# Performance work log

Measured on AMD Instinct MI355X. Metric: run time of the kernel, lower is better.

The kernel has to match this reference:

```python
import jax, jax.numpy as jnp
import numpy as np

TAU = 0.07          # temperature
NUM_CLASSES = 1000  # label vocabulary size (used for bincount length)


def setup_inputs() -> dict:
    key = jax.random.key(0)
    kq, kk, ky = jax.random.split(key, 3)
    N, K, D = 8192, 8, 512
    q = jax.random.normal(kq, (N, D), dtype=jnp.float32)
    q = q / jnp.linalg.norm(q, axis=1, keepdims=True)          # L2-normalized anchors
    k = jax.random.normal(kk, (N, K, D), dtype=jnp.float32)
    k = k / jnp.linalg.norm(k, axis=2, keepdims=True)          # L2-normalized positives
    y = jax.random.randint(ky, (N,), 0, NUM_CLASSES, dtype=jnp.int32)
    return {"q": q, "k": k, "y": y}


def reference(q, k, y):
    # q: [N, D] anchors, k: [N, K, D] external positives, y: [N] labels
    N, K, D = k.shape
    neg_inf = jnp.float32(-jnp.inf)

    # similarities to external positives and within-batch, scaled by temperature
    k_sims = jnp.einsum('nd,nkd->nk', q, k) / TAU            # [N, K]
    batch_sims = jnp.matmul(q, q.T) / TAU                    # [N, N]

    same = y[:, None] == y[None, :]                          # [N, N] label equality
    eye = jnp.eye(N, dtype=bool)
    same_class_mask = same & ~eye                            # in-batch positives (excl. self)
    same_class_counts = same_class_mask.sum(axis=1) + K      # [N]

    # faithful to torch: multiply by mask then masked_fill(x == 0, -inf)
    batch_pos = batch_sims * same_class_mask
    batch_pos = jnp.where(batch_pos == 0, neg_inf, batch_pos)
    pos_sims = jnp.concatenate([k_sims, batch_pos], axis=1)  # [N, K+N]
    num = jax.scipy.special.logsumexp(pos_sims, axis=1)      # [N]

    y_counts = jnp.bincount(y, length=NUM_CLASSES)           # [C]
    neg_sims = batch_sims * (~same)
    neg_sims = jnp.where(neg_sims == 0, neg_inf, neg_sims)
    # class-frequency-weighted denominator (as in the original, no max-shift)
    den = jnp.log(jnp.sum(jnp.exp(neg_sims) / y_counts[y][None, :].astype(q.dtype), axis=1))

    loss = -(num - den) / same_class_counts.astype(q.dtype)
    return loss.mean()
```

## Files before the change

kernel.cpp:

```cpp
#include <hip/hip_runtime.h>
#include <hip/hip_fp8.h>
#include <stdint.h>

constexpr int N    = 8192;
constexpr int D    = 512;
constexpr int KEXT = 8;
constexpr int NCLS = 1000;
#define TAU_INV  14.285714285714285714f
#define SQRT_TI  3.7796447300922722f

typedef long   long2_t __attribute__((ext_vector_type(2)));
typedef float  f32x4   __attribute__((ext_vector_type(4)));

typedef __attribute__((address_space(1))) void gvoid;
typedef __attribute__((address_space(3))) void lvoid;

__device__ __forceinline__ uint32_t pack4_e4m3(float a, float b, float c, float d) {
    __hip_fp8_e4m3 A(a), B(b), C(c), D(d);
    return (uint32_t)A.__x | ((uint32_t)B.__x << 8) |
           ((uint32_t)C.__x << 16) | ((uint32_t)D.__x << 24);
}

__global__ void prep_k(const float* __restrict__ q, const int* __restrict__ y,
                       uint32_t* __restrict__ qf8, int* __restrict__ counts,
                       float* __restrict__ invy, float* __restrict__ pos,
                       float* __restrict__ neg) {
    const int b = blockIdx.x, tid = threadIdx.x;
    if (b == 0) {
        __shared__ int h[NCLS];
        for (int i = tid; i < NCLS; i += 256) h[i] = 0;
        __syncthreads();
        for (int i = tid; i < N; i += 256) atomicAdd(&h[y[i]], 1);
        __syncthreads();
        for (int i = tid; i < NCLS; i += 256) counts[i] = h[i];
        for (int i = tid; i < N; i += 256) invy[i] = 1.0f / (float)h[y[i]];
        return;
    }
    const int gid = (b - 1) * 256 + tid;
    const int row = gid >> 5;
    const int c   = gid & 31;
    const int ks2 = c >> 2, quad = c & 3;
    const float* src = q + (size_t)row * D + ks2 * 64 + quad * 8;
    float4 v0 = *reinterpret_cast<const float4*>(src);
    float4 v1 = *reinterpret_cast<const float4*>(src + 4);
    float4 v2 = *reinterpret_cast<const float4*>(src + 32);
    float4 v3 = *reinterpret_cast<const float4*>(src + 36);
    uint4 o;
    o.x = pack4_e4m3(v0.x * SQRT_TI, v0.y * SQRT_TI, v0.z * SQRT_TI, v0.w * SQRT_TI);
    o.y = pack4_e4m3(v1.x * SQRT_TI, v1.y * SQRT_TI, v1.z * SQRT_TI, v1.w * SQRT_TI);
    o.z = pack4_e4m3(v2.x * SQRT_TI, v2.y * SQRT_TI, v2.z * SQRT_TI, v2.w * SQRT_TI);
    o.w = pack4_e4m3(v3.x * SQRT_TI, v3.y * SQRT_TI, v3.z * SQRT_TI, v3.w * SQRT_TI);
    const int t = row >> 4, l15 = row & 15;
    reinterpret_cast<uint4*>(qf8)[(size_t)t * 512 + ks2 * 64 + quad * 16 + l15] = o;
    if (gid < N) { pos[gid] = 0.f; neg[gid] = 0.f; }
}

__global__ __launch_bounds__(256, 2) void gemm_k(
        const uint32_t* __restrict__ qf8,
        const int* __restrict__ y,
        const float* __restrict__ invy,
        float* __restrict__ pos_sum,
        float* __restrict__ neg_sum) {
    __shared__ long2_t Asl[4096];
    __shared__ int   yR[128];
    __shared__ float redP[2][128];
    __shared__ float redN[2][128];

    const int tid  = threadIdx.x;
    const int wave = tid >> 6;
    const int lane = tid & 63;
    const int quad = lane >> 4;
    const int l15  = lane & 15;

    const int ib     = blockIdx.x >> 3;
    const int jchunk = blockIdx.x & 7;
    const int ibase  = ib * 128;

    {
        const uint32_t* src = qf8 + (size_t)ib * 16384;
#pragma unroll
        for (int it = 0; it < 16; it++) {
            const int idx = it * 256 + tid;
            __builtin_amdgcn_global_load_lds((gvoid*)(src + idx * 4),
                                             (lvoid*)(Asl + idx), 16, 0, 0);
        }
    }
    if (tid < 128) yR[tid] = y[ibase + tid];
    __syncthreads();

    const int wr = (wave >> 1) * 64;
    const int wc = (wave & 1) * 64;
    const int half = wave & 1;

    float posp[16], negp[16];
#pragma unroll
    for (int e = 0; e < 16; e++) { posp[e] = 0.f; negp[e] = 0.f; }

    const long2_t* fb = reinterpret_cast<const long2_t*>(qf8);
    const long2_t* pB[4];
#pragma unroll
    for (int m = 0; m < 4; m++)
        pB[m] = fb + (size_t)(jchunk * 64 + (wc >> 4) + m) * 512 + lane;

    const long2_t* As = Asl + (wr >> 4) * 512 + lane;

    for (int jt = 0; jt < 8; jt++) {
        const int j0 = jchunk * 1024 + jt * 128;

        int   yjv[4];
        float icj[4];
#pragma unroll
        for (int mj = 0; mj < 4; mj++) {
            int jc = j0 + wc + mj * 16 + l15;
            yjv[mj] = y[jc];
            icj[mj] = invy[jc];
        }

        f32x4 acc[4][4];
#pragma unroll
        for (int a = 0; a < 4; a++)
#pragma unroll
            for (int c = 0; c < 4; c++) acc[a][c] = (f32x4)0.0f;

        long2_t bf[2][4];
#pragma unroll
        for (int m = 0; m < 4; m++) bf[0][m] = pB[m][0];

#pragma unroll
        for (int ks2 = 0; ks2 < 8; ks2++) {
            const int cur = ks2 & 1, nxt = cur ^ 1;
            if (ks2 < 7) {
#pragma unroll
                for (int m = 0; m < 4; m++) bf[nxt][m] = pB[m][(ks2 + 1) * 64];
            }
            long2_t af[4];
#pragma unroll
            for (int m = 0; m < 4; m++) af[m] = As[m * 512 + ks2 * 64];
#pragma unroll
            for (int mi = 0; mi < 4; mi++)
#pragma unroll
                for (int mj = 0; mj < 4; mj++)
                    acc[mi][mj] = __builtin_amdgcn_mfma_f32_16x16x32_fp8_fp8(
                        af[mi].x, bf[cur][mj].x, acc[mi][mj], 0, 0, 0);
#pragma unroll
            for (int mi = 0; mi < 4; mi++)
#pragma unroll
                for (int mj = 0; mj < 4; mj++)
                    acc[mi][mj] = __builtin_amdgcn_mfma_f32_16x16x32_fp8_fp8(
                        af[mi].y, bf[cur][mj].y, acc[mi][mj], 0, 0, 0);
        }
#pragma unroll
        for (int m = 0; m < 4; m++) pB[m] += 4096;

#pragma unroll
        for (int mi = 0; mi < 4; mi++) {
#pragma unroll
            for (int r = 0; r < 4; r++) {
                const int il   = wr + mi * 16 + quad * 4 + r;
                const int irow = ibase + il;
                const int myi  = yR[il];
                float ps = 0.f, ns = 0.f;
#pragma unroll
                for (int mj = 0; mj < 4; mj++) {
                    const int jcol = j0 + wc + mj * 16 + l15;
                    float a    = acc[mi][mj][r];
                    float ex   = __expf(a);
                    bool  nz   = (a != 0.0f);
                    bool  same = (myi == yjv[mj]);
                    ps += (same && (irow != jcol) && nz) ? ex : 0.0f;
                    ns += (!same && nz) ? ex * icj[mj] : 0.0f;
                }
                posp[mi * 4 + r] += ps;
                negp[mi * 4 + r] += ns;
            }
        }
    }

#pragma unroll
    for (int mi = 0; mi < 4; mi++) {
#pragma unroll
        for (int r = 0; r < 4; r++) {
            const int e = mi * 4 + r;
            float ps = posp[e], ns = negp[e];
#pragma unroll
            for (int off = 1; off < 16; off <<= 1) {
                ps += __shfl_xor(ps, off);
                ns += __shfl_xor(ns, off);
            }
            if (l15 == 0) {
                const int il = wr + mi * 16 + quad * 4 + r;
                redP[half][il] = ps;
                redN[half][il] = ns;
            }
        }
    }
    __syncthreads();
    if (tid < 128) {
        atomicAdd(&pos_sum[ibase + tid], redP[0][tid] + redP[1][tid]);
    } else if (tid < 256) {
        const int il = tid - 128;
        atomicAdd(&neg_sum[ibase + il], redN[0][il] + redN[1][il]);
    }
}

__global__ void finalize_k(const float* __restrict__ q, const float* __restrict__ kmat,
                           const int* __restrict__ y, const int* __restrict__ counts,
                           const float* __restrict__ pos_sum, const float* __restrict__ neg_sum,
                           float* __restrict__ loss) {
    const int wave = threadIdx.x >> 6, lane = threadIdx.x & 63;
    const int i = blockIdx.x * 4 + wave;

    const float4* q4 = reinterpret_cast<const float4*>(q) + (size_t)i * 128;
    const float4* k4 = reinterpret_cast<const float4*>(kmat) + (size_t)i * KEXT * 128;
    float4 qa = q4[lane], qb = q4[lane + 64];

    float esum = 0.f;
    for (int kk = 0; kk < KEXT; kk++) {
        float4 ka = k4[(size_t)kk * 128 + lane];
        float4 kb = k4[(size_t)kk * 128 + lane + 64];
        float p = qa.x * ka.x;
        p = fmaf(qa.y, ka.y, p); p = fmaf(qa.z, ka.z, p); p = fmaf(qa.w, ka.w, p);
        p = fmaf(qb.x, kb.x, p); p = fmaf(qb.y, kb.y, p);
        p = fmaf(qb.z, kb.z, p); p = fmaf(qb.w, kb.w, p);
#pragma unroll
        for (int off = 1; off < 64; off <<= 1) p += __shfl_xor(p, off);
        esum += __expf(p * TAU_INV);
    }
    if (lane == 0) {
        float num = logf(esum + pos_sum[i]);
        float den = logf(neg_sum[i]);
        float cnt = (float)(counts[y[i]] - 1 + KEXT);
        loss[i] = -(num - den) / cnt;
    }
}

__global__ void reduce_k(const float* __restrict__ loss, float* __restrict__ out) {
    __shared__ float part[16];
    int tid = threadIdx.x;
    float s = 0.f;
    for (int i = tid; i < N; i += 1024) s += loss[i];
#pragma unroll
    for (int off = 1; off < 64; off <<= 1) s += __shfl_xor(s, off);
    if ((tid & 63) == 0) part[tid >> 6] = s;
    __syncthreads();
    if (tid < 16) {
        float v = part[tid];
#pragma unroll
        for (int off = 1; off < 16; off <<= 1) v += __shfl_xor(v, off);
        if (tid == 0) out[0] = v / (float)N;
    }
}

extern "C" void kernel_launch(void* const* d_in, const int* in_sizes, int n_in,
                              void* d_out, int out_size, void* d_ws, size_t ws_size,
                              hipStream_t stream) {
    const float* q    = (const float*)d_in[0];
    const float* kmat = (const float*)d_in[1];
    const int*   y    = (const int*)d_in[2];
    float* out = (float*)d_out;

    char* ws = (char*)d_ws;
    uint32_t* qf8  = (uint32_t*)ws;
    int*   counts  = (int*)  (ws + 4194304);
    float* invy    = (float*)(ws + 4198400);
    float* pos     = (float*)(ws + 4231168);
    float* neg     = (float*)(ws + 4263936);
    float* loss    = (float*)(ws + 4296704);

    prep_k    <<<1 + (N * 32) / 256, 256, 0, stream>>>(q, y, qf8, counts, invy, pos, neg);
    gemm_k    <<<512, 256, 0, stream>>>(qf8, y, invy, pos, neg);
    finalize_k<<<N / 4, 256, 0, stream>>>(q, kmat, y, counts, pos, neg, loss);
    reduce_k  <<<1, 1024, 0, stream>>>(loss, out);
}
```

Baseline: 333.1 us.

## Move same-class positive sums out of GEMM epilogue into sparse finalize pass

The GEMM epilogue now sums every off-diagonal exp weighted by inverse class count, with no label compares and no positive accumulator. Finalize ballots over the labels to find each row's same-class partners and computes their positive similarities in fp32. It also recomputes their fp8 dot products so it can subtract those terms from the negative sum. Adds a deeper register prefetch ring in the GEMM and folds the mean reduction into finalize with an atomic, which drops one launch. The risks are a scan of all 8192 labels per row in finalize and floating-point cancellation in the subtraction.

```diff
diff --git a/kernel.cpp b/kernel.cpp
--- a/kernel.cpp
+++ b/kernel.cpp
@@ -20,11 +20,14 @@
     return (uint32_t)A.__x | ((uint32_t)B.__x << 8) |
            ((uint32_t)C.__x << 16) | ((uint32_t)D.__x << 24);
 }
+__device__ __forceinline__ float f8tof(uint32_t b) {
+    __hip_fp8_e4m3 v; v.__x = (uint8_t)b; return (float)v;
+}
 
 __global__ void prep_k(const float* __restrict__ q, const int* __restrict__ y,
                        uint32_t* __restrict__ qf8, int* __restrict__ counts,
-                       float* __restrict__ invy, float* __restrict__ pos,
-                       float* __restrict__ neg) {
+                       float* __restrict__ invy, float* __restrict__ neg,
+                       float* __restrict__ out) {
     const int b = blockIdx.x, tid = threadIdx.x;
     if (b == 0) {
         __shared__ int h[NCLS];
@@ -33,6 +36,7 @@
         for (int i = tid; i < N; i += 256) atomicAdd(&h[y[i]], 1);
         __syncthreads();
         for (int i = tid; i < NCLS; i += 256) counts[i] = h[i];
+        if (tid == 0) out[0] = 0.f;
         for (int i = tid; i < N; i += 256) invy[i] = 1.0f / (float)h[y[i]];
         return;
     }
@@ -52,18 +56,14 @@
     o.w = pack4_e4m3(v3.x * SQRT_TI, v3.y * SQRT_TI, v3.z * SQRT_TI, v3.w * SQRT_TI);
     const int t = row >> 4, l15 = row & 15;
     reinterpret_cast<uint4*>(qf8)[(size_t)t * 512 + ks2 * 64 + quad * 16 + l15] = o;
-    if (gid < N) { pos[gid] = 0.f; neg[gid] = 0.f; }
+    if (gid < N) neg[gid] = 0.f;
 }
 
 __global__ __launch_bounds__(256, 2) void gemm_k(
         const uint32_t* __restrict__ qf8,
-        const int* __restrict__ y,
         const float* __restrict__ invy,
-        float* __restrict__ pos_sum,
         float* __restrict__ neg_sum) {
     __shared__ long2_t Asl[4096];
-    __shared__ int   yR[128];
-    __shared__ float redP[2][128];
     __shared__ float redN[2][128];
 
     const int tid  = threadIdx.x;
@@ -85,16 +85,15 @@
                                              (lvoid*)(Asl + idx), 16, 0, 0);
         }
     }
-    if (tid < 128) yR[tid] = y[ibase + tid];
     __syncthreads();
 
     const int wr = (wave >> 1) * 64;
     const int wc = (wave & 1) * 64;
     const int half = wave & 1;
 
-    float posp[16], negp[16];
-#pragma unroll
-    for (int e = 0; e < 16; e++) { posp[e] = 0.f; negp[e] = 0.f; }
+    float negp[16];
+#pragma unroll
+    for (int e = 0; e < 16; e++) negp[e] = 0.f;
 
     const long2_t* fb = reinterpret_cast<const long2_t*>(qf8);
     const long2_t* pB[4];
@@ -107,13 +106,12 @@
     for (int jt = 0; jt < 8; jt++) {
         const int j0 = jchunk * 1024 + jt * 128;
 
-        int   yjv[4];
+        int   jc[4];
         float icj[4];
 #pragma unroll
         for (int mj = 0; mj < 4; mj++) {
-            int jc = j0 + wc + mj * 16 + l15;
-            yjv[mj] = y[jc];
-            icj[mj] = invy[jc];
+            jc[mj]  = j0 + wc + mj * 16 + l15;
+            icj[mj] = invy[jc[mj]];
         }
 
         f32x4 acc[4][4];
@@ -122,32 +120,38 @@
 #pragma unroll
             for (int c = 0; c < 4; c++) acc[a][c] = (f32x4)0.0f;
 
-        long2_t bf[2][4];
-#pragma unroll
-        for (int m = 0; m < 4; m++) bf[0][m] = pB[m][0];
-
+        long2_t bf[3][4], af[2][4];
+#pragma unroll
+        for (int m = 0; m < 4; m++) {
+            bf[0][m] = pB[m][0];
+            bf[1][m] = pB[m][64];
+            af[0][m] = As[m * 512];
+        }
 #pragma unroll
         for (int ks2 = 0; ks2 < 8; ks2++) {
-            const int cur = ks2 & 1, nxt = cur ^ 1;
+            const int cur = ks2 % 3;
+            if (ks2 + 2 < 8) {
+                const int ns = (ks2 + 2) % 3;
+#pragma unroll
+                for (int m = 0; m < 4; m++) bf[ns][m] = pB[m][(ks2 + 2) * 64];
+            }
+            const int ac = ks2 & 1;
             if (ks2 < 7) {
 #pragma unroll
-                for (int m = 0; m < 4; m++) bf[nxt][m] = pB[m][(ks2 + 1) * 64];
-            }
-            long2_t af[4];
-#pragma unroll
-            for (int m = 0; m < 4; m++) af[m] = As[m * 512 + ks2 * 64];
+                for (int m = 0; m < 4; m++) af[ac ^ 1][m] = As[m * 512 + (ks2 + 1) * 64];
+            }
 #pragma unroll
             for (int mi = 0; mi < 4; mi++)
 #pragma unroll
                 for (int mj = 0; mj < 4; mj++)
                     acc[mi][mj] = __builtin_amdgcn_mfma_f32_16x16x32_fp8_fp8(
-                        af[mi].x, bf[cur][mj].x, acc[mi][mj], 0, 0, 0);
+                        af[ac][mi].x, bf[cur][mj].x, acc[mi][mj], 0, 0, 0);
 #pragma unroll
             for (int mi = 0; mi < 4; mi++)
 #pragma unroll
                 for (int mj = 0; mj < 4; mj++)
                     acc[mi][mj] = __builtin_amdgcn_mfma_f32_16x16x32_fp8_fp8(
-                        af[mi].y, bf[cur][mj].y, acc[mi][mj], 0, 0, 0);
+                        af[ac][mi].y, bf[cur][mj].y, acc[mi][mj], 0, 0, 0);
         }
 #pragma unroll
         for (int m = 0; m < 4; m++) pB[m] += 4096;
@@ -156,21 +160,14 @@
         for (int mi = 0; mi < 4; mi++) {
 #pragma unroll
             for (int r = 0; r < 4; r++) {
-                const int il   = wr + mi * 16 + quad * 4 + r;
-                const int irow = ibase + il;
-                const int myi  = yR[il];
-                float ps = 0.f, ns = 0.f;
+                const int irow = ibase + wr + mi * 16 + quad * 4 + r;
+                float ns = 0.f;
 #pragma unroll
                 for (int mj = 0; mj < 4; mj++) {
-                    const int jcol = j0 + wc + mj * 16 + l15;
-                    float a    = acc[mi][mj][r];
-                    float ex   = __expf(a);
-                    bool  nz   = (a != 0.0f);
-                    bool  same = (myi == yjv[mj]);
-                    ps += (same && (irow != jcol) && nz) ? ex : 0.0f;
-                    ns += (!same && nz) ? ex * icj[mj] : 0.0f;
+                    float ex = __expf(acc[mi][mj][r]);
+                    ex = (irow == jc[mj]) ? 0.f : ex;
+                    ns = fmaf(ex, icj[mj], ns);
                 }
-                posp[mi * 4 + r] += ps;
                 negp[mi * 4 + r] += ns;
             }
         }
@@ -180,44 +177,34 @@
     for (int mi = 0; mi < 4; mi++) {
 #pragma unroll
         for (int r = 0; r < 4; r++) {
-            const int e = mi * 4 + r;
-            float ps = posp[e], ns = negp[e];
-#pragma unroll
-            for (int off = 1; off < 16; off <<= 1) {
-                ps += __shfl_xor(ps, off);
-                ns += __shfl_xor(ns, off);
-            }
-            if (l15 == 0) {
-                const int il = wr + mi * 16 + quad * 4 + r;
-                redP[half][il] = ps;
-                redN[half][il] = ns;
-            }
+            float ns = negp[mi * 4 + r];
+#pragma unroll
+            for (int off = 1; off < 16; off <<= 1) ns += __shfl_xor(ns, off);
+            if (l15 == 0) redN[half][wr + mi * 16 + quad * 4 + r] = ns;
         }
     }
     __syncthreads();
-    if (tid < 128) {
-        atomicAdd(&pos_sum[ibase + tid], redP[0][tid] + redP[1][tid]);
-    } else if (tid < 256) {
-        const int il = tid - 128;
-        atomicAdd(&neg_sum[ibase + il], redN[0][il] + redN[1][il]);
-    }
+    if (tid < 128)
+        atomicAdd(&neg_sum[ibase + tid], redN[0][tid] + redN[1][tid]);
 }
 
 __global__ void finalize_k(const float* __restrict__ q, const float* __restrict__ kmat,
                            const int* __restrict__ y, const int* __restrict__ counts,
-                           const float* __restrict__ pos_sum, const float* __restrict__ neg_sum,
-                           float* __restrict__ loss) {
+                           const float* __restrict__ neg_sum,
+                           const uint32_t* __restrict__ qf8,
+                           float* __restrict__ out) {
+    __shared__ float part[4];
     const int wave = threadIdx.x >> 6, lane = threadIdx.x & 63;
     const int i = blockIdx.x * 4 + wave;
 
-    const float4* q4 = reinterpret_cast<const float4*>(q) + (size_t)i * 128;
+    const float4* q4 = reinterpret_cast<const float4*>(q);
+    float4 qa = q4[(size_t)i * 128 + lane], qb = q4[(size_t)i * 128 + 64 + lane];
+
     const float4* k4 = reinterpret_cast<const float4*>(kmat) + (size_t)i * KEXT * 128;
-    float4 qa = q4[lane], qb = q4[lane + 64];
-
     float esum = 0.f;
     for (int kk = 0; kk < KEXT; kk++) {
         float4 ka = k4[(size_t)kk * 128 + lane];
-        float4 kb = k4[(size_t)kk * 128 + lane + 64];
+        float4 kb = k4[(size_t)kk * 128 + 64 + lane];
         float p = qa.x * ka.x;
         p = fmaf(qa.y, ka.y, p); p = fmaf(qa.z, ka.z, p); p = fmaf(qa.w, ka.w, p);
         p = fmaf(qb.x, kb.x, p); p = fmaf(qb.y, kb.y, p);
@@ -226,29 +213,63 @@
         for (int off = 1; off < 64; off <<= 1) p += __shfl_xor(p, off);
         esum += __expf(p * TAU_INV);
     }
+
+    const uint4* f4 = reinterpret_cast<const uint4*>(qf8);
+    const bool act = lane < 32;
+    const int ks2 = lane >> 2, quad = lane & 3;
+    const size_t goff = (size_t)ks2 * 64 + quad * 16;
+    uint4 iv = act ? f4[(size_t)(i >> 4) * 512 + goff + (i & 15)] : uint4{0, 0, 0, 0};
+    float fi[16];
+#pragma unroll
+    for (int w = 0; w < 4; w++) {
+        uint32_t word = (&iv.x)[w];
+#pragma unroll
+        for (int t = 0; t < 4; t++) fi[w * 4 + t] = f8tof((word >> (8 * t)) & 0xffu);
+    }
+
+    const int myy = y[i];
+    float pos = 0.f, corr = 0.f;
+    for (int it = 0; it < 128; it++) {
+        unsigned long long m = __ballot(y[it * 64 + lane] == myy);
+        if (it == (i >> 6)) m &= ~(1ull << (i & 63));
+        while (m) {
+            const int b = __builtin_ctzll(m); m &= m - 1;
+            const int j = it * 64 + b;
+            float4 ja = q4[(size_t)j * 128 + lane], jb = q4[(size_t)j * 128 + 64 + lane];
+            float p = qa.x * ja.x;
+            p = fmaf(qa.y, ja.y, p); p = fmaf(qa.z, ja.z, p); p = fmaf(qa.w, ja.w, p);
+            p = fmaf(qb.x, jb.x, p); p = fmaf(qb.y, jb.y, p);
+            p = fmaf(qb.z, jb.z, p); p = fmaf(qb.w, jb.w, p);
+            uint4 jv = act ? f4[(size_t)(j >> 4) * 512 + goff + (j & 15)] : uint4{0, 0, 0, 0};
+            float p8 = 0.f;
+#pragma unroll
+            for (int w = 0; w < 4; w++) {
+                uint32_t word = (&jv.x)[w];
+#pragma unroll
+                for (int t = 0; t < 4; t++)
+                    p8 = fmaf(fi[w * 4 + t], f8tof((word >> (8 * t)) & 0xffu), p8);
+            }
+#pragma unroll
+            for (int off = 1; off < 64; off <<= 1) {
+                p  += __shfl_xor(p, off);
+                p8 += __shfl_xor(p8, off);
+            }
+            pos  += __expf(p * TAU_INV);
+            corr += __expf(p8);
+        }
+    }
+
     if (lane == 0) {
-        float num = logf(esum + pos_sum[i]);
-        float den = logf(neg_sum[i]);
-        float cnt = (float)(counts[y[i]] - 1 + KEXT);
-        loss[i] = -(num - den) / cnt;
-    }
-}
-
-__global__ void reduce_k(const float* __restrict__ loss, float* __restrict__ out) {
-    __shared__ float part[16];
-    int tid = threadIdx.x;
-    float s = 0.f;
-    for (int i = tid; i < N; i += 1024) s += loss[i];
-#pragma unroll
-    for (int off = 1; off < 64; off <<= 1) s += __shfl_xor(s, off);
-    if ((tid & 63) == 0) part[tid >> 6] = s;
+        const float ici = 1.0f / (float)counts[myy];
+        float den_sum = neg_sum[i] - corr * ici;
+        float num = logf(esum + pos);
+        float den = logf(den_sum);
+        float cnt = (float)(counts[myy] - 1 + KEXT);
+        part[wave] = -(num - den) / (cnt * (float)N);
+    }
     __syncthreads();
-    if (tid < 16) {
-        float v = part[tid];
-#pragma unroll
-        for (int off = 1; off < 16; off <<= 1) v += __shfl_xor(v, off);
-        if (tid == 0) out[0] = v / (float)N;
-    }
+    if (threadIdx.x == 0)
+        atomicAdd(out, part[0] + part[1] + part[2] + part[3]);
 }
 
 extern "C" void kernel_launch(void* const* d_in, const int* in_sizes, int n_in,
@@ -263,12 +284,9 @@
     uint32_t* qf8  = (uint32_t*)ws;
     int*   counts  = (int*)  (ws + 4194304);
     float* invy    = (float*)(ws + 4198400);
-    float* pos     = (float*)(ws + 4231168);
-    float* neg     = (float*)(ws + 4263936);
-    float* loss    = (float*)(ws + 4296704);
-
-    prep_k    <<<1 + (N * 32) / 256, 256, 0, stream>>>(q, y, qf8, counts, invy, pos, neg);
-    gemm_k    <<<512, 256, 0, stream>>>(qf8, y, invy, pos, neg);
-    finalize_k<<<N / 4, 256, 0, stream>>>(q, kmat, y, counts, pos, neg, loss);
-    reduce_k  <<<1, 1024, 0, stream>>>(loss, out);
-}
+    float* neg     = (float*)(ws + 4231168);
+
+    prep_k    <<<1 + (N * 32) / 256, 256, 0, stream>>>(q, y, qf8, counts, invy, neg, out);
+    gemm_k    <<<512, 256, 0, stream>>>(qf8, invy, neg);
+    finalize_k<<<N / 4, 256, 0, stream>>>(q, kmat, y, counts, neg, qf8, out);
+}
```

Result: slower. 342.0 us (+2.7%).
